# Kernel tuning notes

Measured on AMD Instinct MI355X. Metric: run time of the kernel, lower is better.

## Reference

```python
import jax, jax.numpy as jnp
import numpy as np

N_NODES = 50000
N_EDGES = 800000
D = 64
L = 2
EPS = 1e-9


def setup_inputs() -> dict:
    key = jax.random.key(0)
    ks = jax.random.split(key, 8)
    node_feats = jax.random.normal(ks[0], (N_NODES, D), dtype=jnp.float32)
    edge_src = jax.random.randint(ks[1], (N_EDGES,), 0, N_NODES, dtype=jnp.int32)
    edge_dst = jnp.sort(jax.random.randint(ks[2], (N_EDGES,), 0, N_NODES, dtype=jnp.int32))
    edge_w = jax.random.uniform(ks[3], (N_EDGES,), dtype=jnp.float32)
    W0 = jax.random.normal(ks[4], (D, D), dtype=jnp.float32) / np.sqrt(D)
    b0 = jax.random.normal(ks[5], (D,), dtype=jnp.float32) * 0.02
    W1 = jax.random.normal(ks[6], (D, D), dtype=jnp.float32) / np.sqrt(D)
    b1 = jax.random.normal(ks[7], (D,), dtype=jnp.float32) * 0.02
    return {"node_feats": node_feats, "edge_src": edge_src, "edge_dst": edge_dst,
            "edge_w": edge_w, "W0": W0, "b0": b0, "W1": W1, "b1": b1}


def reference(node_feats, edge_src, edge_dst, edge_w, W0, b0, W1, b1):
    n = node_feats.shape[0]
    # per-destination normalizer: sum of incoming edge weights + eps
    denom = jax.ops.segment_sum(edge_w, edge_dst, num_segments=n) + EPS  # [N]
    feats = node_feats
    for _ in range(L):
        # gather neighbor feats, weight, scatter-add to destination, normalize
        weighted = edge_w[:, None] * feats[edge_src]                      # [E, D]
        msg = jax.ops.segment_sum(weighted, edge_dst, num_segments=n)     # [N, D]
        msg = msg / denom[:, None]
        feats = jax.nn.relu(feats @ W0.T + b0 + msg @ W1.T + b1)
        # isolated nodes: segment_sum gives 0 -> msg = 0, matching msg=0.0 in torch
    return feats
```

## Files before the change

kernel.cpp:

```cpp
#include <hip/hip_runtime.h>

#define D 64
#define EPSV 1e-9f

typedef __attribute__((ext_vector_type(8))) short bf8_t;
typedef __attribute__((ext_vector_type(4))) float f4_t;

__device__ inline float bf2f(short u) {
    union { unsigned int i; float f; } v;
    v.i = ((unsigned int)(unsigned short)u) << 16;
    return v.f;
}
__device__ inline unsigned short f2bf(float f) {
    union { float f; unsigned int i; } v; v.f = f;
    unsigned int r = v.i + 0x7fff + ((v.i >> 16) & 1);
    return (unsigned short)(r >> 16);
}

__global__ void prep_kernel(const float* __restrict__ node_feats,
                            const int*   __restrict__ edge_dst,
                            const float* __restrict__ W0,
                            const float* __restrict__ W1,
                            int* __restrict__ row_off,
                            unsigned short* __restrict__ Wpack,
                            unsigned short* __restrict__ XA,
                            unsigned short* __restrict__ XB,
                            int n_nodes, int n_edges, int cvtb)
{
    const int bid = blockIdx.x;
    const int tid = threadIdx.x;
    if (bid < cvtb) {
        const int i = bid * 256 + tid;
        if (i < n_nodes * 16) {
            const float4 v = ((const float4*)node_feats)[i];
            const int row = i >> 4, c4 = (i & 15) * 4;
            unsigned short* p = (c4 < 32) ? (XA + row * 32 + c4)
                                          : (XB + row * 32 + (c4 - 32));
            p[0] = f2bf(v.x); p[1] = f2bf(v.y); p[2] = f2bf(v.z); p[3] = f2bf(v.w);
        }
    } else if (bid < cvtb + 32) {
        const int idx = (bid - cvtb) * 256 + tid;
        const int j = idx & 7, lane = (idx >> 3) & 63, kk = (idx >> 9) & 3, t = idx >> 11;
        const int k = kk * 32 + (lane >> 4) * 8 + j;
        const int d = t * 16 + (lane & 15);
        const float v = (k < D) ? W0[d * D + k] : W1[d * D + (k - D)];
        Wpack[idx] = f2bf(v);
    } else {
        const int i = (bid - cvtb - 32) * 256 + tid;
        if (i <= n_edges) {
            const int prev = (i == 0) ? -1 : edge_dst[i - 1];
            const int cur  = (i == n_edges) ? n_nodes : edge_dst[i];
            for (int n = prev + 1; n <= cur; ++n) row_off[n] = i;
        }
    }
}

__global__ __launch_bounds__(256, 8) void aggregate_kernel(
    const unsigned short* __restrict__ XA,
    const unsigned short* __restrict__ XB,
    unsigned short* __restrict__ M,
    const int*   __restrict__ row_off,
    const int*   __restrict__ edge_src,
    const float* __restrict__ edge_w,
    int n_nodes)
{
    const int lane  = threadIdx.x & 63;
    const int wib   = threadIdx.x >> 6;
    const int chunk = blockIdx.x & 1;
    const unsigned short* __restrict__ P = chunk ? XB : XA;

    const int h  = lane >> 5;
    int node = (blockIdx.x >> 1) * 8 + wib * 2 + h;
    if (node >= n_nodes) node = n_nodes - 1;

    const int s = row_off[node];
    const int e = row_off[node + 1];
    const int deg = e - s;
    const int od  = __shfl_xor(deg, 32);
    const int degmax = deg > od ? deg : od;

    const int sid = (lane >> 2) & 7;
    const int fo  = (lane & 3) * 8;

    float acc[8];
    #pragma unroll
    for (int m = 0; m < 8; ++m) acc[m] = 0.f;
    float wsum = 0.f;

    #pragma unroll
    for (int g = 0; g < 2; ++g) {
        const int  ej = s + g * 8 + sid;
        const bool v  = ej < e;
        const float w = v ? edge_w[ej] : 0.f;
        const int  sc = v ? edge_src[ej] : 0;
        const bf8_t f = *(const bf8_t*)(P + sc * 32 + fo);
        #pragma unroll
        for (int m = 0; m < 8; ++m) acc[m] = fmaf(w, bf2f(f[m]), acc[m]);
        wsum += w;
    }
    if (degmax > 16) {
        #pragma unroll
        for (int g = 2; g < 4; ++g) {
            const int  ej = s + g * 8 + sid;
            const bool v  = ej < e;
            const float w = v ? edge_w[ej] : 0.f;
            const int  sc = v ? edge_src[ej] : 0;
            const bf8_t f = *(const bf8_t*)(P + sc * 32 + fo);
            #pragma unroll
            for (int m = 0; m < 8; ++m) acc[m] = fmaf(w, bf2f(f[m]), acc[m]);
            wsum += w;
        }
    }
    for (int base = 32; base < degmax; base += 8) {
        const int  ej = s + base + sid;
        const bool v  = ej < e;
        const float w = v ? edge_w[ej] : 0.f;
        const int  sc = v ? edge_src[ej] : 0;
        const bf8_t f = *(const bf8_t*)(P + sc * 32 + fo);
        #pragma unroll
        for (int m = 0; m < 8; ++m) acc[m] = fmaf(w, bf2f(f[m]), acc[m]);
        wsum += w;
    }

    #pragma unroll
    for (int off = 4; off <= 16; off <<= 1) {
        #pragma unroll
        for (int m = 0; m < 8; ++m) acc[m] += __shfl_xor(acc[m], off);
        wsum += __shfl_xor(wsum, off);
    }

    const float inv = 1.0f / (wsum + EPSV);
    if ((lane & 28) == 0) {
        bf8_t mv;
        #pragma unroll
        for (int m = 0; m < 8; ++m) mv[m] = (short)f2bf(acc[m] * inv);
        *(bf8_t*)(M + node * 64 + chunk * 32 + fo) = mv;
    }
}

template<int OUT_F32>
__global__ __launch_bounds__(256, 4) void gemm_mfma(
    const unsigned short* __restrict__ XA,
    const unsigned short* __restrict__ XB,
    const unsigned short* __restrict__ M,
    const unsigned short* __restrict__ Wpack,
    const float* __restrict__ b0,
    const float* __restrict__ b1,
    void* __restrict__ outA,
    void* __restrict__ outB,
    int ntiles, int waves_total, int n_nodes)
{
    const int lane = threadIdx.x & 63;
    const int wib  = threadIdx.x >> 6;
    const int wave = __builtin_amdgcn_readfirstlane(blockIdx.x * 4 + wib);

    bf8_t bfr[4][4];
    #pragma unroll
    for (int t = 0; t < 4; ++t)
        #pragma unroll
        for (int kk = 0; kk < 4; ++kk)
            bfr[t][kk] = *(const bf8_t*)(Wpack + ((t * 4 + kk) * 64 + lane) * 8);

    float bias[4];
    #pragma unroll
    for (int t = 0; t < 4; ++t) {
        const int col = t * 16 + (lane & 15);
        bias[t] = b0[col] + b1[col];
    }

    const int koff = (lane >> 4) * 8;

    for (int tile = wave; tile < ntiles; tile += waves_total) {
        const int rowbase = tile * 16;
        int arow = rowbase + (lane & 15); if (arow >= n_nodes) arow = n_nodes - 1;

        bf8_t af[4];
        af[0] = *(const bf8_t*)(XA + arow * 32 + koff);
        af[1] = *(const bf8_t*)(XB + arow * 32 + koff);
        af[2] = *(const bf8_t*)(M + arow * 64 + koff);
        af[3] = *(const bf8_t*)(M + arow * 64 + 32 + koff);

        f4_t acc[4];
        #pragma unroll
        for (int t = 0; t < 4; ++t) acc[t] = (f4_t){0.f, 0.f, 0.f, 0.f};

        #pragma unroll
        for (int t = 0; t < 4; ++t)
            #pragma unroll
            for (int kk = 0; kk < 4; ++kk)
                acc[t] = __builtin_amdgcn_mfma_f32_16x16x32_bf16(af[kk], bfr[t][kk], acc[t], 0, 0, 0);

        #pragma unroll
        for (int t = 0; t < 4; ++t) {
            const int col = t * 16 + (lane & 15);
            #pragma unroll
            for (int r = 0; r < 4; ++r) {
                const int row = rowbase + (lane >> 4) * 4 + r;
                if (row < n_nodes) {
                    const float v = fmaxf(acc[t][r] + bias[t], 0.0f);
                    if (OUT_F32) {
                        ((float*)outA)[row * 64 + col] = v;
                    } else {
                        if (col < 32) ((unsigned short*)outA)[row * 32 + col] = f2bf(v);
                        else          ((unsigned short*)outB)[row * 32 + col - 32] = f2bf(v);
                    }
                }
            }
        }
    }
}

extern "C" void kernel_launch(void* const* d_in, const int* in_sizes, int n_in,
                              void* d_out, int out_size, void* d_ws, size_t ws_size,
                              hipStream_t stream) {
    const float* node_feats = (const float*)d_in[0];
    const int*   edge_src   = (const int*)  d_in[1];
    const int*   edge_dst   = (const int*)  d_in[2];
    const float* edge_w     = (const float*)d_in[3];
    const float* W0         = (const float*)d_in[4];
    const float* b0         = (const float*)d_in[5];
    const float* W1         = (const float*)d_in[6];
    const float* b1         = (const float*)d_in[7];

    const int n_nodes = in_sizes[0] / D;
    const int n_edges = in_sizes[1];

    char* ws = (char*)d_ws;
    int*            row_off = (int*)ws;
    unsigned short* Wpack   = (unsigned short*)(ws + 204800);
    const size_t base = 237568;
    unsigned short* XA0 = (unsigned short*)(ws + base);
    unsigned short* XB0 = (unsigned short*)(ws + base + 3200000);
    unsigned short* XA1 = (unsigned short*)(ws + base + 6400000);
    unsigned short* XB1 = (unsigned short*)(ws + base + 9600000);
    unsigned short* M   = (unsigned short*)(ws + base + 12800000);

    const int cvtb = (n_nodes * 16 + 255) / 256;
    const int offb = (n_edges + 1 + 255) / 256;
    prep_kernel<<<cvtb + 32 + offb, 256, 0, stream>>>(node_feats, edge_dst, W0, W1,
                                                      row_off, Wpack, XA0, XB0,
                                                      n_nodes, n_edges, cvtb);

    const int agrid  = 2 * ((n_nodes + 7) / 8);
    const int ntiles = (n_nodes + 15) / 16;
    const int ggrid  = 256;
    const int gwaves = ggrid * 4;

    aggregate_kernel<<<agrid, 256, 0, stream>>>(XA0, XB0, M, row_off, edge_src, edge_w, n_nodes);
    gemm_mfma<0><<<ggrid, 256, 0, stream>>>(XA0, XB0, M, Wpack, b0, b1,
                                            XA1, XB1, ntiles, gwaves, n_nodes);
    aggregate_kernel<<<agrid, 256, 0, stream>>>(XA1, XB1, M, row_off, edge_src, edge_w, n_nodes);
    gemm_mfma<1><<<ggrid, 256, 0, stream>>>(XA1, XB1, M, Wpack, b0, b1,
                                            d_out, nullptr, ntiles, gwaves, n_nodes);
}
```

Measured before the change: 74.24 us.

## Merge split feature halves into one row-major bf16 buffer and batch gathers

After: 61.91 us (median of 2 runs). 1.2x faster.

```diff
diff --git a/kernel.cpp b/kernel.cpp
--- a/kernel.cpp
+++ b/kernel.cpp
@@ -23,8 +23,7 @@
                             const float* __restrict__ W1,
                             int* __restrict__ row_off,
                             unsigned short* __restrict__ Wpack,
-                            unsigned short* __restrict__ XA,
-                            unsigned short* __restrict__ XB,
+                            unsigned short* __restrict__ X,
                             int n_nodes, int n_edges, int cvtb)
 {
     const int bid = blockIdx.x;
@@ -34,8 +33,7 @@
         if (i < n_nodes * 16) {
             const float4 v = ((const float4*)node_feats)[i];
             const int row = i >> 4, c4 = (i & 15) * 4;
-            unsigned short* p = (c4 < 32) ? (XA + row * 32 + c4)
-                                          : (XB + row * 32 + (c4 - 32));
+            unsigned short* p = X + row * 64 + c4;
             p[0] = f2bf(v.x); p[1] = f2bf(v.y); p[2] = f2bf(v.z); p[3] = f2bf(v.w);
         }
     } else if (bid < cvtb + 32) {
@@ -56,21 +54,17 @@
 }
 
 __global__ __launch_bounds__(256, 8) void aggregate_kernel(
-    const unsigned short* __restrict__ XA,
-    const unsigned short* __restrict__ XB,
+    const unsigned short* __restrict__ X,
     unsigned short* __restrict__ M,
     const int*   __restrict__ row_off,
     const int*   __restrict__ edge_src,
     const float* __restrict__ edge_w,
     int n_nodes)
 {
-    const int lane  = threadIdx.x & 63;
-    const int wib   = threadIdx.x >> 6;
-    const int chunk = blockIdx.x & 1;
-    const unsigned short* __restrict__ P = chunk ? XB : XA;
-
-    const int h  = lane >> 5;
-    int node = (blockIdx.x >> 1) * 8 + wib * 2 + h;
+    const int lane = threadIdx.x & 63;
+    const int wib  = threadIdx.x >> 6;
+    const int h    = lane >> 5;
+    int node = blockIdx.x * 8 + wib * 2 + h;
     if (node >= n_nodes) node = n_nodes - 1;
 
     const int s = row_off[node];
@@ -79,80 +73,102 @@
     const int od  = __shfl_xor(deg, 32);
     const int degmax = deg > od ? deg : od;
 
-    const int sid = (lane >> 2) & 7;
-    const int fo  = (lane & 3) * 8;
+    const int slot = (lane >> 3) & 3;
+    const int fo   = (lane & 7) * 8;
 
     float acc[8];
     #pragma unroll
     for (int m = 0; m < 8; ++m) acc[m] = 0.f;
     float wsum = 0.f;
 
-    #pragma unroll
-    for (int g = 0; g < 2; ++g) {
-        const int  ej = s + g * 8 + sid;
-        const bool v  = ej < e;
-        const float w = v ? edge_w[ej] : 0.f;
-        const int  sc = v ? edge_src[ej] : 0;
-        const bf8_t f = *(const bf8_t*)(P + sc * 32 + fo);
-        #pragma unroll
-        for (int m = 0; m < 8; ++m) acc[m] = fmaf(w, bf2f(f[m]), acc[m]);
-        wsum += w;
+    {
+        float w[4]; int sc[4];
+        #pragma unroll
+        for (int r = 0; r < 4; ++r) {
+            const int  ej = s + r * 4 + slot;
+            const bool v  = ej < e;
+            w[r]  = v ? edge_w[ej] : 0.f;
+            sc[r] = v ? edge_src[ej] : 0;
+        }
+        bf8_t f[4];
+        #pragma unroll
+        for (int r = 0; r < 4; ++r) f[r] = *(const bf8_t*)(X + sc[r] * 64 + fo);
+        #pragma unroll
+        for (int r = 0; r < 4; ++r) {
+            #pragma unroll
+            for (int m = 0; m < 8; ++m) acc[m] = fmaf(w[r], bf2f(f[r][m]), acc[m]);
+            wsum += w[r];
+        }
     }
     if (degmax > 16) {
-        #pragma unroll
-        for (int g = 2; g < 4; ++g) {
-            const int  ej = s + g * 8 + sid;
+        float w[4]; int sc[4];
+        #pragma unroll
+        for (int r = 0; r < 4; ++r) {
+            const int  ej = s + 16 + r * 4 + slot;
             const bool v  = ej < e;
-            const float w = v ? edge_w[ej] : 0.f;
-            const int  sc = v ? edge_src[ej] : 0;
-            const bf8_t f = *(const bf8_t*)(P + sc * 32 + fo);
+            w[r]  = v ? edge_w[ej] : 0.f;
+            sc[r] = v ? edge_src[ej] : 0;
+        }
+        bf8_t f[4];
+        #pragma unroll
+        for (int r = 0; r < 4; ++r) f[r] = *(const bf8_t*)(X + sc[r] * 64 + fo);
+        #pragma unroll
+        for (int r = 0; r < 4; ++r) {
             #pragma unroll
-            for (int m = 0; m < 8; ++m) acc[m] = fmaf(w, bf2f(f[m]), acc[m]);
-            wsum += w;
-        }
-    }
-    for (int base = 32; base < degmax; base += 8) {
-        const int  ej = s + base + sid;
-        const bool v  = ej < e;
-        const float w = v ? edge_w[ej] : 0.f;
-        const int  sc = v ? edge_src[ej] : 0;
-        const bf8_t f = *(const bf8_t*)(P + sc * 32 + fo);
-        #pragma unroll
-        for (int m = 0; m < 8; ++m) acc[m] = fmaf(w, bf2f(f[m]), acc[m]);
-        wsum += w;
-    }
-
-    #pragma unroll
-    for (int off = 4; off <= 16; off <<= 1) {
+            for (int m = 0; m < 8; ++m) acc[m] = fmaf(w[r], bf2f(f[r][m]), acc[m]);
+            wsum += w[r];
+        }
+    }
+    for (int base = 32; base < degmax; base += 16) {
+        float w[4]; int sc[4];
+        #pragma unroll
+        for (int r = 0; r < 4; ++r) {
+            const int  ej = s + base + r * 4 + slot;
+            const bool v  = ej < e;
+            w[r]  = v ? edge_w[ej] : 0.f;
+            sc[r] = v ? edge_src[ej] : 0;
+        }
+        bf8_t f[4];
+        #pragma unroll
+        for (int r = 0; r < 4; ++r) f[r] = *(const bf8_t*)(X + sc[r] * 64 + fo);
+        #pragma unroll
+        for (int r = 0; r < 4; ++r) {
+            #pragma unroll
+            for (int m = 0; m < 8; ++m) acc[m] = fmaf(w[r], bf2f(f[r][m]), acc[m]);
+            wsum += w[r];
+        }
+    }
+
+    #pragma unroll
+    for (int off = 8; off <= 16; off <<= 1) {
         #pragma unroll
         for (int m = 0; m < 8; ++m) acc[m] += __shfl_xor(acc[m], off);
         wsum += __shfl_xor(wsum, off);
     }
 
     const float inv = 1.0f / (wsum + EPSV);
-    if ((lane & 28) == 0) {
+    if (slot == 0) {
         bf8_t mv;
         #pragma unroll
         for (int m = 0; m < 8; ++m) mv[m] = (short)f2bf(acc[m] * inv);
-        *(bf8_t*)(M + node * 64 + chunk * 32 + fo) = mv;
+        *(bf8_t*)(M + node * 64 + fo) = mv;
     }
 }
 
 template<int OUT_F32>
 __global__ __launch_bounds__(256, 4) void gemm_mfma(
-    const unsigned short* __restrict__ XA,
-    const unsigned short* __restrict__ XB,
+    const unsigned short* __restrict__ X,
     const unsigned short* __restrict__ M,
     const unsigned short* __restrict__ Wpack,
     const float* __restrict__ b0,
     const float* __restrict__ b1,
-    void* __restrict__ outA,
-    void* __restrict__ outB,
-    int ntiles, int waves_total, int n_nodes)
+    void* __restrict__ outp,
+    int ntiles, int n_nodes)
 {
     const int lane = threadIdx.x & 63;
     const int wib  = threadIdx.x >> 6;
-    const int wave = __builtin_amdgcn_readfirstlane(blockIdx.x * 4 + wib);
+    const int tile = __builtin_amdgcn_readfirstlane(blockIdx.x * 4 + wib);
+    if (tile >= ntiles) return;
 
     bf8_t bfr[4][4];
     #pragma unroll
@@ -169,42 +185,35 @@
     }
 
     const int koff = (lane >> 4) * 8;
-
-    for (int tile = wave; tile < ntiles; tile += waves_total) {
-        const int rowbase = tile * 16;
-        int arow = rowbase + (lane & 15); if (arow >= n_nodes) arow = n_nodes - 1;
-
-        bf8_t af[4];
-        af[0] = *(const bf8_t*)(XA + arow * 32 + koff);
-        af[1] = *(const bf8_t*)(XB + arow * 32 + koff);
-        af[2] = *(const bf8_t*)(M + arow * 64 + koff);
-        af[3] = *(const bf8_t*)(M + arow * 64 + 32 + koff);
-
-        f4_t acc[4];
-        #pragma unroll
-        for (int t = 0; t < 4; ++t) acc[t] = (f4_t){0.f, 0.f, 0.f, 0.f};
-
-        #pragma unroll
-        for (int t = 0; t < 4; ++t)
-            #pragma unroll
-            for (int kk = 0; kk < 4; ++kk)
-                acc[t] = __builtin_amdgcn_mfma_f32_16x16x32_bf16(af[kk], bfr[t][kk], acc[t], 0, 0, 0);
-
-        #pragma unroll
-        for (int t = 0; t < 4; ++t) {
-            const int col = t * 16 + (lane & 15);
-            #pragma unroll
-            for (int r = 0; r < 4; ++r) {
-                const int row = rowbase + (lane >> 4) * 4 + r;
-                if (row < n_nodes) {
-                    const float v = fmaxf(acc[t][r] + bias[t], 0.0f);
-                    if (OUT_F32) {
-                        ((float*)outA)[row * 64 + col] = v;
-                    } else {
-                        if (col < 32) ((unsigned short*)outA)[row * 32 + col] = f2bf(v);
-                        else          ((unsigned short*)outB)[row * 32 + col - 32] = f2bf(v);
-                    }
-                }
+    const int rowbase = tile * 16;
+    int arow = rowbase + (lane & 15); if (arow >= n_nodes) arow = n_nodes - 1;
+
+    bf8_t af[4];
+    af[0] = *(const bf8_t*)(X + arow * 64 + koff);
+    af[1] = *(const bf8_t*)(X + arow * 64 + 32 + koff);
+    af[2] = *(const bf8_t*)(M + arow * 64 + koff);
+    af[3] = *(const bf8_t*)(M + arow * 64 + 32 + koff);
+
+    f4_t acc[4];
+    #pragma unroll
+    for (int t = 0; t < 4; ++t) acc[t] = (f4_t){0.f, 0.f, 0.f, 0.f};
+
+    #pragma unroll
+    for (int t = 0; t < 4; ++t)
+        #pragma unroll
+        for (int kk = 0; kk < 4; ++kk)
+            acc[t] = __builtin_amdgcn_mfma_f32_16x16x32_bf16(af[kk], bfr[t][kk], acc[t], 0, 0, 0);
+
+    #pragma unroll
+    for (int t = 0; t < 4; ++t) {
+        const int col = t * 16 + (lane & 15);
+        #pragma unroll
+        for (int r = 0; r < 4; ++r) {
+            const int row = rowbase + (lane >> 4) * 4 + r;
+            if (row < n_nodes) {
+                const float v = fmaxf(acc[t][r] + bias[t], 0.0f);
+                if (OUT_F32) ((float*)outp)[row * 64 + col] = v;
+                else         ((unsigned short*)outp)[row * 64 + col] = f2bf(v);
             }
         }
     }
@@ -229,27 +238,22 @@
     int*            row_off = (int*)ws;
     unsigned short* Wpack   = (unsigned short*)(ws + 204800);
     const size_t base = 237568;
-    unsigned short* XA0 = (unsigned short*)(ws + base);
-    unsigned short* XB0 = (unsigned short*)(ws + base + 3200000);
-    unsigned short* XA1 = (unsigned short*)(ws + base + 6400000);
-    unsigned short* XB1 = (unsigned short*)(ws + base + 9600000);
-    unsigned short* M   = (unsigned short*)(ws + base + 12800000);
+    unsigned short* X0 = (unsigned short*)(ws + base);
+    unsigned short* X1 = (unsigned short*)(ws + base + 6400000);
+    unsigned short* M  = (unsigned short*)(ws + base + 12800000);
 
     const int cvtb = (n_nodes * 16 + 255) / 256;
     const int offb = (n_edges + 1 + 255) / 256;
     prep_kernel<<<cvtb + 32 + offb, 256, 0, stream>>>(node_feats, edge_dst, W0, W1,
-                                                      row_off, Wpack, XA0, XB0,
+                                                      row_off, Wpack, X0,
                                                       n_nodes, n_edges, cvtb);
 
-    const int agrid  = 2 * ((n_nodes + 7) / 8);
+    const int agrid  = (n_nodes + 7) / 8;
     const int ntiles = (n_nodes + 15) / 16;
-    const int ggrid  = 256;
-    const int gwaves = ggrid * 4;
-
-    aggregate_kernel<<<agrid, 256, 0, stream>>>(XA0, XB0, M, row_off, edge_src, edge_w, n_nodes);
-    gemm_mfma<0><<<ggrid, 256, 0, stream>>>(XA0, XB0, M, Wpack, b0, b1,
-                                            XA1, XB1, ntiles, gwaves, n_nodes);
-    aggregate_kernel<<<agrid, 256, 0, stream>>>(XA1, XB1, M, row_off, edge_src, edge_w, n_nodes);
-    gemm_mfma<1><<<ggrid, 256, 0, stream>>>(XA1, XB1, M, Wpack, b0, b1,
-                                            d_out, nullptr, ntiles, gwaves, n_nodes);
-}
+    const int ggrid  = (ntiles + 3) / 4;
+
+    aggregate_kernel<<<agrid, 256, 0, stream>>>(X0, M, row_off, edge_src, edge_w, n_nodes);
+    gemm_mfma<0><<<ggrid, 256, 0, stream>>>(X0, M, Wpack, b0, b1, X1, ntiles, n_nodes);
+    aggregate_kernel<<<agrid, 256, 0, stream>>>(X1, M, row_off, edge_src, edge_w, n_nodes);
+    gemm_mfma<1><<<ggrid, 256, 0, stream>>>(X1, M, Wpack, b0, b1, d_out, ntiles, n_nodes);
+}
```

## Use persistent grid-stride aggregation and one-tile-per-wave GEMM launch

Applied to the files above, without the earlier changes.

New measurement: 93.59 us. 1.26x slower.

```diff
diff --git a/kernel.cpp b/kernel.cpp
--- a/kernel.cpp
+++ b/kernel.cpp
@@ -27,8 +27,7 @@
                             unsigned short* __restrict__ XB,
                             int n_nodes, int n_edges, int cvtb)
 {
-    const int bid = blockIdx.x;
-    const int tid = threadIdx.x;
+    const int bid = blockIdx.x, tid = threadIdx.x;
     if (bid < cvtb) {
         const int i = bid * 256 + tid;
         if (i < n_nodes * 16) {
@@ -62,79 +61,108 @@
     const int*   __restrict__ row_off,
     const int*   __restrict__ edge_src,
     const float* __restrict__ edge_w,
-    int n_nodes)
+    int n_nodes, int nwaves_c)
 {
     const int lane  = threadIdx.x & 63;
     const int wib   = threadIdx.x >> 6;
-    const int chunk = blockIdx.x & 1;
+    const int b     = blockIdx.x;
+    const int chunk = b & 1;
     const unsigned short* __restrict__ P = chunk ? XB : XA;
 
-    const int h  = lane >> 5;
-    int node = (blockIdx.x >> 1) * 8 + wib * 2 + h;
-    if (node >= n_nodes) node = n_nodes - 1;
-
-    const int s = row_off[node];
-    const int e = row_off[node + 1];
-    const int deg = e - s;
-    const int od  = __shfl_xor(deg, 32);
-    const int degmax = deg > od ? deg : od;
-
+    const int h   = lane >> 5;
     const int sid = (lane >> 2) & 7;
     const int fo  = (lane & 3) * 8;
 
-    float acc[8];
-    #pragma unroll
-    for (int m = 0; m < 8; ++m) acc[m] = 0.f;
-    float wsum = 0.f;
-
-    #pragma unroll
-    for (int g = 0; g < 2; ++g) {
-        const int  ej = s + g * 8 + sid;
-        const bool v  = ej < e;
-        const float w = v ? edge_w[ej] : 0.f;
-        const int  sc = v ? edge_src[ej] : 0;
-        const bf8_t f = *(const bf8_t*)(P + sc * 32 + fo);
-        #pragma unroll
-        for (int m = 0; m < 8; ++m) acc[m] = fmaf(w, bf2f(f[m]), acc[m]);
-        wsum += w;
-    }
-    if (degmax > 16) {
-        #pragma unroll
-        for (int g = 2; g < 4; ++g) {
-            const int  ej = s + g * 8 + sid;
-            const bool v  = ej < e;
-            const float w = v ? edge_w[ej] : 0.f;
-            const int  sc = v ? edge_src[ej] : 0;
-            const bf8_t f = *(const bf8_t*)(P + sc * 32 + fo);
-            #pragma unroll
-            for (int m = 0; m < 8; ++m) acc[m] = fmaf(w, bf2f(f[m]), acc[m]);
-            wsum += w;
-        }
-    }
-    for (int base = 32; base < degmax; base += 8) {
-        const int  ej = s + base + sid;
-        const bool v  = ej < e;
-        const float w = v ? edge_w[ej] : 0.f;
-        const int  sc = v ? edge_src[ej] : 0;
-        const bf8_t f = *(const bf8_t*)(P + sc * 32 + fo);
-        #pragma unroll
-        for (int m = 0; m < 8; ++m) acc[m] = fmaf(w, bf2f(f[m]), acc[m]);
-        wsum += w;
-    }
-
-    #pragma unroll
-    for (int off = 4; off <= 16; off <<= 1) {
-        #pragma unroll
-        for (int m = 0; m < 8; ++m) acc[m] += __shfl_xor(acc[m], off);
-        wsum += __shfl_xor(wsum, off);
-    }
-
-    const float inv = 1.0f / (wsum + EPSV);
-    if ((lane & 28) == 0) {
-        bf8_t mv;
-        #pragma unroll
-        for (int m = 0; m < 8; ++m) mv[m] = (short)f2bf(acc[m] * inv);
-        *(bf8_t*)(M + node * 64 + chunk * 32 + fo) = mv;
+    const int wave_c = (b >> 1) * 4 + wib;
+    const int ntasks = (n_nodes + 1) / 2;
+
+    for (int task = wave_c; task < ntasks; task += nwaves_c) {
+        int node = task * 2 + h;
+        if (node >= n_nodes) node = n_nodes - 1;
+
+        const int s = row_off[node];
+        const int e = row_off[node + 1];
+        const int deg = e - s;
+        const int od  = __shfl_xor(deg, 32);
+        const int degmax = deg > od ? deg : od;
+
+        float acc[8];
+        #pragma unroll
+        for (int m = 0; m < 8; ++m) acc[m] = 0.f;
+        float wsum = 0.f;
+
+        {
+            float w[2]; int sc[2];
+            #pragma unroll
+            for (int g = 0; g < 2; ++g) {
+                const int  ej = s + g * 8 + sid;
+                const bool v  = ej < e;
+                w[g]  = v ? __builtin_nontemporal_load(edge_w + ej) : 0.f;
+                sc[g] = v ? __builtin_nontemporal_load(edge_src + ej) : 0;
+            }
+            bf8_t f[2];
+            #pragma unroll
+            for (int g = 0; g < 2; ++g) f[g] = *(const bf8_t*)(P + sc[g] * 32 + fo);
+            #pragma unroll
+            for (int g = 0; g < 2; ++g) {
+                #pragma unroll
+                for (int m = 0; m < 8; ++m) acc[m] = fmaf(w[g], bf2f(f[g][m]), acc[m]);
+                wsum += w[g];
+            }
+        }
+        if (degmax > 16) {
+            float w[2]; int sc[2];
+            #pragma unroll
+            for (int g = 0; g < 2; ++g) {
+                const int  ej = s + 16 + g * 8 + sid;
+                const bool v  = ej < e;
+                w[g]  = v ? __builtin_nontemporal_load(edge_w + ej) : 0.f;
+                sc[g] = v ? __builtin_nontemporal_load(edge_src + ej) : 0;
+            }
+            bf8_t f[2];
+            #pragma unroll
+            for (int g = 0; g < 2; ++g) f[g] = *(const bf8_t*)(P + sc[g] * 32 + fo);
+            #pragma unroll
+            for (int g = 0; g < 2; ++g) {
+                #pragma unroll
+                for (int m = 0; m < 8; ++m) acc[m] = fmaf(w[g], bf2f(f[g][m]), acc[m]);
+                wsum += w[g];
+            }
+        }
+        for (int base = 32; base < degmax; base += 16) {
+            float w[2]; int sc[2];
+            #pragma unroll
+            for (int g = 0; g < 2; ++g) {
+                const int  ej = s + base + g * 8 + sid;
+                const bool v  = ej < e;
+                w[g]  = v ? __builtin_nontemporal_load(edge_w + ej) : 0.f;
+                sc[g] = v ? __builtin_nontemporal_load(edge_src + ej) : 0;
+            }
+            bf8_t f[2];
+            #pragma unroll
+            for (int g = 0; g < 2; ++g) f[g] = *(const bf8_t*)(P + sc[g] * 32 + fo);
+            #pragma unroll
+            for (int g = 0; g < 2; ++g) {
+                #pragma unroll
+                for (int m = 0; m < 8; ++m) acc[m] = fmaf(w[g], bf2f(f[g][m]), acc[m]);
+                wsum += w[g];
+            }
+        }
+
+        #pragma unroll
+        for (int off = 4; off <= 16; off <<= 1) {
+            #pragma unroll
+            for (int m = 0; m < 8; ++m) acc[m] += __shfl_xor(acc[m], off);
+            wsum += __shfl_xor(wsum, off);
+        }
+
+        const float inv = 1.0f / (wsum + EPSV);
+        if (sid == 0) {
+            bf8_t mv;
+            #pragma unroll
+            for (int m = 0; m < 8; ++m) mv[m] = (short)f2bf(acc[m] * inv);
+            __builtin_nontemporal_store(mv, (bf8_t*)(M + node * 64 + chunk * 32 + fo));
+        }
     }
 }
 
@@ -148,11 +176,12 @@
     const float* __restrict__ b1,
     void* __restrict__ outA,
     void* __restrict__ outB,
-    int ntiles, int waves_total, int n_nodes)
+    int ntiles, int n_nodes)
 {
     const int lane = threadIdx.x & 63;
     const int wib  = threadIdx.x >> 6;
-    const int wave = __builtin_amdgcn_readfirstlane(blockIdx.x * 4 + wib);
+    const int tile = __builtin_amdgcn_readfirstlane(blockIdx.x * 4 + wib);
+    if (tile >= ntiles) return;
 
     bf8_t bfr[4][4];
     #pragma unroll
@@ -169,41 +198,38 @@
     }
 
     const int koff = (lane >> 4) * 8;
-
-    for (int tile = wave; tile < ntiles; tile += waves_total) {
-        const int rowbase = tile * 16;
-        int arow = rowbase + (lane & 15); if (arow >= n_nodes) arow = n_nodes - 1;
-
-        bf8_t af[4];
-        af[0] = *(const bf8_t*)(XA + arow * 32 + koff);
-        af[1] = *(const bf8_t*)(XB + arow * 32 + koff);
-        af[2] = *(const bf8_t*)(M + arow * 64 + koff);
-        af[3] = *(const bf8_t*)(M + arow * 64 + 32 + koff);
-
-        f4_t acc[4];
-        #pragma unroll
-        for (int t = 0; t < 4; ++t) acc[t] = (f4_t){0.f, 0.f, 0.f, 0.f};
-
-        #pragma unroll
-        for (int t = 0; t < 4; ++t)
-            #pragma unroll
-            for (int kk = 0; kk < 4; ++kk)
-                acc[t] = __builtin_amdgcn_mfma_f32_16x16x32_bf16(af[kk], bfr[t][kk], acc[t], 0, 0, 0);
-
-        #pragma unroll
-        for (int t = 0; t < 4; ++t) {
-            const int col = t * 16 + (lane & 15);
-            #pragma unroll
-            for (int r = 0; r < 4; ++r) {
-                const int row = rowbase + (lane >> 4) * 4 + r;
-                if (row < n_nodes) {
-                    const float v = fmaxf(acc[t][r] + bias[t], 0.0f);
-                    if (OUT_F32) {
-                        ((float*)outA)[row * 64 + col] = v;
-                    } else {
-                        if (col < 32) ((unsigned short*)outA)[row * 32 + col] = f2bf(v);
-                        else          ((unsigned short*)outB)[row * 32 + col - 32] = f2bf(v);
-                    }
+    const int rowbase = tile * 16;
+    int arow = rowbase + (lane & 15); if (arow >= n_nodes) arow = n_nodes - 1;
+
+    bf8_t af[4];
+    af[0] = *(const bf8_t*)(XA + arow * 32 + koff);
+    af[1] = *(const bf8_t*)(XB + arow * 32 + koff);
+    af[2] = *(const bf8_t*)(M + arow * 64 + koff);
+    af[3] = *(const bf8_t*)(M + arow * 64 + 32 + koff);
+
+    f4_t acc[4];
+    #pragma unroll
+    for (int t = 0; t < 4; ++t) acc[t] = (f4_t){0.f, 0.f, 0.f, 0.f};
+
+    #pragma unroll
+    for (int t = 0; t < 4; ++t)
+        #pragma unroll
+        for (int kk = 0; kk < 4; ++kk)
+            acc[t] = __builtin_amdgcn_mfma_f32_16x16x32_bf16(af[kk], bfr[t][kk], acc[t], 0, 0, 0);
+
+    #pragma unroll
+    for (int t = 0; t < 4; ++t) {
+        const int col = t * 16 + (lane & 15);
+        #pragma unroll
+        for (int r = 0; r < 4; ++r) {
+            const int row = rowbase + (lane >> 4) * 4 + r;
+            if (row < n_nodes) {
+                const float v = fmaxf(acc[t][r] + bias[t], 0.0f);
+                if (OUT_F32) {
+                    ((float*)outA)[row * 64 + col] = v;
+                } else {
+                    if (col < 32) ((unsigned short*)outA)[row * 32 + col] = f2bf(v);
+                    else          ((unsigned short*)outB)[row * 32 + col - 32] = f2bf(v);
                 }
             }
         }
@@ -241,15 +267,26 @@
                                                       row_off, Wpack, XA0, XB0,
                                                       n_nodes, n_edges, cvtb);
 
-    const int agrid  = 2 * ((n_nodes + 7) / 8);
+    int numCU = 304, maxB = 8, dev = 0;
+    hipGetDevice(&dev);
+    hipDeviceGetAttribute(&numCU, hipDeviceAttributeMultiprocessorCount, dev);
+    hipOccupancyMaxActiveBlocksPerMultiprocessor(&maxB, (const void*)aggregate_kernel, 256, 0);
+    if (maxB < 1) maxB = 1;
+    int agrid = numCU * maxB;
+    if (agrid > 4096) agrid = 4096;
+    agrid &= ~1;
+    if (agrid < 2) agrid = 2;
+    const int nwaves_c = (agrid / 2) * 4;
+
     const int ntiles = (n_nodes + 15) / 16;
-    const int ggrid  = 256;
-    const int gwaves = ggrid * 4;
-
-    aggregate_kernel<<<agrid, 256, 0, stream>>>(XA0, XB0, M, row_off, edge_src, edge_w, n_nodes);
+    const int ggrid  = (ntiles + 3) / 4;
+
+    aggregate_kernel<<<agrid, 256, 0, stream>>>(XA0, XB0, M, row_off, edge_src, edge_w,
+                                                n_nodes, nwaves_c);
     gemm_mfma<0><<<ggrid, 256, 0, stream>>>(XA0, XB0, M, Wpack, b0, b1,
-                                            XA1, XB1, ntiles, gwaves, n_nodes);
-    aggregate_kernel<<<agrid, 256, 0, stream>>>(XA1, XB1, M, row_off, edge_src, edge_w, n_nodes);
+                                            XA1, XB1, ntiles, n_nodes);
+    aggregate_kernel<<<agrid, 256, 0, stream>>>(XA1, XB1, M, row_off, edge_src, edge_w,
+                                                n_nodes, nwaves_c);
     gemm_mfma<1><<<ggrid, 256, 0, stream>>>(XA1, XB1, M, Wpack, b0, b1,
-                                            d_out, nullptr, ntiles, gwaves, n_nodes);
-}
+                                            d_out, nullptr, ntiles, n_nodes);
+}
```
